# Optimization experiments

Measured on AMD Instinct MI355X. Metric: run time of the kernel, lower is better.

Reference implementation:

```python
import jax, jax.numpy as jnp
import numpy as np

D = 1024      # input_dim / hidden_size
H = 16        # n_heads
HD = D // H   # head_size = 64
F = 4096      # mlp_dim
EPS = 1e-6


def setup_inputs() -> dict:
    key = jax.random.key(0)
    ks = jax.random.split(key, 16)
    s = 0.02
    inp = {
        "x": jax.random.normal(ks[0], (4, 2048, D), dtype=jnp.float32),
        # attention params (torch Linear: y = x @ W.T + b; we store W as [out,in])
        "Wq": jax.random.normal(ks[1], (D, D), dtype=jnp.float32) * s,
        "bq": jax.random.normal(ks[2], (D,), dtype=jnp.float32) * s,
        "Wk": jax.random.normal(ks[3], (D, D), dtype=jnp.float32) * s,
        "bk": jax.random.normal(ks[4], (D,), dtype=jnp.float32) * s,
        "Wv": jax.random.normal(ks[5], (D, D), dtype=jnp.float32) * s,
        "bv": jax.random.normal(ks[6], (D,), dtype=jnp.float32) * s,
        "Wo": jax.random.normal(ks[7], (D, D), dtype=jnp.float32) * s,
        "bo": jax.random.normal(ks[8], (D,), dtype=jnp.float32) * s,
        # MLP params
        "W1": jax.random.normal(ks[9], (F, D), dtype=jnp.float32) * s,
        "b1": jax.random.normal(ks[10], (F,), dtype=jnp.float32) * s,
        "W2": jax.random.normal(ks[11], (D, F), dtype=jnp.float32) * s,
        "b2": jax.random.normal(ks[12], (D,), dtype=jnp.float32) * s,
        # LayerNorm params
        "ln1_g": jnp.ones((D,), dtype=jnp.float32),
        "ln1_b": jnp.zeros((D,), dtype=jnp.float32),
        "ln2_g": jnp.ones((D,), dtype=jnp.float32),
        "ln2_b": jnp.zeros((D,), dtype=jnp.float32),
    }
    return inp


def _layernorm(x, g, b):
    mu = jnp.mean(x, axis=-1, keepdims=True)
    var = jnp.mean(jnp.square(x - mu), axis=-1, keepdims=True)
    return (x - mu) * jax.lax.rsqrt(var + EPS) * g + b


def reference(x, Wq, bq, Wk, bk, Wv, bv, Wo, bo, W1, b1, W2, b2,
              ln1_g, ln1_b, ln2_g, ln2_b):
    B, S, _ = x.shape
    h = x
    xn = _layernorm(x, ln1_g, ln1_b)
    # Q/K/V projections -> [B, H, S, HD]
    def split_heads(t):
        return t.reshape(B, S, H, HD).transpose(0, 2, 1, 3)
    q = split_heads(xn @ Wq.T + bq)
    k = split_heads(xn @ Wk.T + bk)
    v = split_heads(xn @ Wv.T + bv)
    scores = jnp.einsum('bhqd,bhkd->bhqk', q, k) / np.sqrt(HD).astype(np.float32)
    probs = jax.nn.softmax(scores, axis=-1)
    ctx = jnp.einsum('bhqk,bhkd->bhqd', probs, v)      # [B,H,S,HD]
    ctx = ctx.transpose(0, 2, 1, 3).reshape(B, S, D)
    attn_out = ctx @ Wo.T + bo
    x = attn_out + h
    h = x
    xn = _layernorm(x, ln2_g, ln2_b)
    y = jax.nn.gelu(xn @ W1.T + b1, approximate=False)  # torch nn.GELU() = exact erf gelu
    y = y @ W2.T + b2
    return y + h
```

## Files before the change

kernel.cpp:

```cpp
#include <hip/hip_runtime.h>
#include <hip/hip_bf16.h>
#include <math.h>

typedef __attribute__((ext_vector_type(8))) short short8;
typedef __attribute__((ext_vector_type(4))) float f32x4;

#define MFMA_BF16 __builtin_amdgcn_mfma_f32_16x16x32_bf16

__device__ __forceinline__ ushort f2bf(float f) {
  union { __hip_bfloat16 h; ushort u; } c;
  c.h = __float2bfloat16(f);
  return c.u;
}
__device__ __forceinline__ void async_cp16(const ushort* g, ushort* l) {
  __builtin_amdgcn_global_load_lds(
      (const __attribute__((address_space(1))) void*)g,
      (__attribute__((address_space(3))) void*)l, 16, 0, 0);
}

__global__ __launch_bounds__(256) void conv_all(
    const float* __restrict__ Wq, const float* __restrict__ Wk,
    const float* __restrict__ Wv, const float* __restrict__ Wo,
    const float* __restrict__ W1, const float* __restrict__ W2,
    const float* __restrict__ bq, const float* __restrict__ bk,
    const float* __restrict__ bv,
    ushort* __restrict__ wqkv, ushort* __restrict__ wo,
    ushort* __restrict__ w1, ushort* __restrict__ w2,
    float* __restrict__ bqkv) {
  int i = blockIdx.x * 256 + threadIdx.x;
  if (i < 3145728) {
    const float* src; ushort* dst; int off;
    if (i < 786432)        {
      dst = wqkv; off = i;
      if (i < 262144)      src = Wq + (size_t)i * 4;
      else if (i < 524288) src = Wk + (size_t)(i - 262144) * 4;
      else                 src = Wv + (size_t)(i - 524288) * 4;
    } else if (i < 1048576) { dst = wo; off = i - 786432;  src = Wo + (size_t)off * 4; }
    else if (i < 2097152)   { dst = w1; off = i - 1048576; src = W1 + (size_t)off * 4; }
    else                    { dst = w2; off = i - 2097152; src = W2 + (size_t)off * 4; }
    float4 v = *(const float4*)src;
    ushort4 o;
    o.x = f2bf(v.x); o.y = f2bf(v.y); o.z = f2bf(v.z); o.w = f2bf(v.w);
    ((ushort4*)dst)[off] = o;
  } else if (i < 3146496) {
    int off = i - 3145728;
    const float* src;
    if (off < 256)      src = bq + (size_t)off * 4;
    else if (off < 512) src = bk + (size_t)(off - 256) * 4;
    else                src = bv + (size_t)(off - 512) * 4;
    ((float4*)bqkv)[off] = *(const float4*)src;
  }
}

__global__ __launch_bounds__(256) void ln_kernel(const float* __restrict__ x,
    const float* __restrict__ g, const float* __restrict__ b,
    ushort* __restrict__ out) {
  const int row = blockIdx.x, t = threadIdx.x;
  float4 v = ((const float4*)(x + (size_t)row * 1024))[t];
  float s  = v.x + v.y + v.z + v.w;
  float ss = v.x*v.x + v.y*v.y + v.z*v.z + v.w*v.w;
  #pragma unroll
  for (int off = 32; off >= 1; off >>= 1) {
    s  += __shfl_xor(s, off);
    ss += __shfl_xor(ss, off);
  }
  __shared__ float red[8];
  int wv = t >> 6, ln = t & 63;
  if (ln == 0) { red[wv] = s; red[4 + wv] = ss; }
  __syncthreads();
  float S  = red[0] + red[1] + red[2] + red[3];
  float SS = red[4] + red[5] + red[6] + red[7];
  float mu  = S * (1.0f/1024.0f);
  float var = SS * (1.0f/1024.0f) - mu*mu;
  float rs  = rsqrtf(var + 1e-6f);
  float4 gv = ((const float4*)g)[t];
  float4 bv = ((const float4*)b)[t];
  ushort4 o;
  o.x = f2bf((v.x-mu)*rs*gv.x + bv.x);
  o.y = f2bf((v.y-mu)*rs*gv.y + bv.y);
  o.z = f2bf((v.z-mu)*rs*gv.z + bv.z);
  o.w = f2bf((v.w-mu)*rs*gv.w + bv.w);
  ((ushort4*)(out + (size_t)row*1024))[t] = o;
}

enum { EPI_QK = 0, EPI_VT = 1, EPI_WO = 2, EPI_GELU = 3, EPI_OUT = 4 };

template <int EPI>
__global__ __launch_bounds__(256) void gemm_kernel(const ushort* __restrict__ A,
    const ushort* __restrict__ Bw, const float* __restrict__ bias,
    const float* __restrict__ res, void* __restrict__ outp,
    void* __restrict__ outp2, int K, int N, float scale) {
  __shared__ ushort As[2][128 * 32];
  __shared__ ushort Bs[2][128 * 32];
  const int t = threadIdx.x;
  const int m0 = blockIdx.x * 128, n0 = blockIdx.y * 128;
  const int lane = t & 63, wave = t >> 6;
  const int col = lane & 15, quad = lane >> 4;
  const int wrow = (wave >> 1) * 64, wcol = (wave & 1) * 64;

  f32x4 acc[4][4];
  #pragma unroll
  for (int i = 0; i < 4; i++)
    #pragma unroll
    for (int j = 0; j < 4; j++)
      acc[i][j] = (f32x4){0.f, 0.f, 0.f, 0.f};

  const int lrow = lane >> 2, lcol = (lane & 3) * 8;
  const ushort* Ag = A  + (size_t)(m0 + wave * 32 + lrow) * K + lcol;
  const ushort* Bg = Bw + (size_t)(n0 + wave * 32 + lrow) * K + lcol;
  const int ldso = (wave * 32) * 32;

  for (int k0 = 0; k0 < K; k0 += 64) {
    __syncthreads();
    #pragma unroll
    for (int c = 0; c < 2; c++) {
      async_cp16(Ag + k0 + c * 32,                  &As[c][ldso]);
      async_cp16(Ag + (size_t)16 * K + k0 + c * 32, &As[c][ldso + 16 * 32]);
      async_cp16(Bg + k0 + c * 32,                  &Bs[c][ldso]);
      async_cp16(Bg + (size_t)16 * K + k0 + c * 32, &Bs[c][ldso + 16 * 32]);
    }
    __syncthreads();
    #pragma unroll
    for (int c = 0; c < 2; c++) {
      short8 af[4], bf[4];
      #pragma unroll
      for (int tm = 0; tm < 4; tm++)
        af[tm] = *(const short8*)&As[c][(wrow + tm * 16 + col) * 32 + quad * 8];
      #pragma unroll
      for (int tn = 0; tn < 4; tn++)
        bf[tn] = *(const short8*)&Bs[c][(wcol + tn * 16 + col) * 32 + quad * 8];
      #pragma unroll
      for (int tm = 0; tm < 4; tm++)
        #pragma unroll
        for (int tn = 0; tn < 4; tn++)
          acc[tm][tn] = MFMA_BF16(af[tm], bf[tn], acc[tm][tn], 0, 0, 0);
    }
  }

  #pragma unroll
  for (int tm = 0; tm < 4; tm++) {
    #pragma unroll
    for (int tn = 0; tn < 4; tn++) {
      const int n = n0 + wcol + tn * 16 + col;
      const float bn = (EPI == EPI_VT) ? 0.f : bias[n];
      #pragma unroll
      for (int r = 0; r < 4; r++) {
        const int m = m0 + wrow + tm * 16 + quad * 4 + r;
        float v = acc[tm][tn][r] + bn;
        if (EPI == EPI_VT) {
          float vv = v + bias[m];
          int h = m >> 6, hd = m & 63, bb = n >> 11, s2 = n & 2047;
          ((ushort*)outp)[((size_t)((bb * 16 + h) * 64 + hd)) * 2048 + s2] = f2bf(vv);
        } else if (EPI == EPI_GELU) {
          float u = v * 0.7978845608028654f * (1.0f + 0.044715f * v * v);
          float e = __builtin_amdgcn_exp2f(u * 2.885390081777927f);
          float th = 1.0f - 2.0f * __builtin_amdgcn_rcpf(e + 1.0f);
          ((ushort*)outp)[(size_t)m * N + n] = f2bf(0.5f * v * (1.0f + th));
        } else {
          ((float*)outp)[(size_t)m * N + n] = v + res[(size_t)m * N + n];
        }
      }
    }
  }
}

template <int EPI>
__global__ __launch_bounds__(512, 2) void gemm256_kernel(const ushort* __restrict__ A,
    const ushort* __restrict__ Bw, const float* __restrict__ bias,
    void* __restrict__ outp, void* __restrict__ outp2, int K, int N, float scale) {
  __shared__ ushort As[2][256 * 64];
  __shared__ ushort Bs[2][256 * 64];
  const int t = threadIdx.x;
  const int lane = t & 63, wave = t >> 6;
  const int col = lane & 15, quad = lane >> 4;
  const int m0 = blockIdx.x * 256, n0 = blockIdx.y * 256;
  const int wm = wave >> 2, wn = wave & 3;

  f32x4 acc[8][4];
  #pragma unroll
  for (int i = 0; i < 8; i++)
    #pragma unroll
    for (int j = 0; j < 4; j++)
      acc[i][j] = (f32x4){0.f, 0.f, 0.f, 0.f};

  size_t aoff[2], boff[2];
  int d0[2];
  #pragma unroll
  for (int i = 0; i < 2; i++) {
    int c = i * 512 + t, r = c >> 3, p = c & 7;
    aoff[i] = (size_t)(m0 + r) * K + (p ^ (r & 7)) * 8;
    boff[i] = (size_t)(n0 + r) * K + (p ^ (r & 7)) * 8;
    d0[i] = c * 8;
  }
  const size_t up = (size_t)128 * K;

  const int NT = K >> 6;
  #pragma unroll
  for (int i = 0; i < 2; i++) async_cp16(A  + aoff[i],      &As[0][d0[i]]);
  #pragma unroll
  for (int i = 0; i < 2; i++) async_cp16(Bw + boff[i],      &Bs[0][d0[i]]);
  #pragma unroll
  for (int i = 0; i < 2; i++) async_cp16(A  + aoff[i] + up, &As[0][8192 + d0[i]]);
  #pragma unroll
  for (int i = 0; i < 2; i++) async_cp16(Bw + boff[i] + up, &Bs[0][8192 + d0[i]]);
  asm volatile("s_waitcnt vmcnt(4)" ::: "memory");
  __builtin_amdgcn_sched_barrier(0);
  __builtin_amdgcn_s_barrier();
  __builtin_amdgcn_sched_barrier(0);

  short8 af[4][2], bf[2][2];
  for (int kt = 0; kt < NT; kt++) {
    const int cur = kt & 1, nxt = cur ^ 1;
    const size_t ko = (size_t)(kt + 1) << 6;
    const bool more = (kt + 1 < NT);
    #pragma unroll
    for (int ph = 0; ph < 4; ph++) {
      const int ha = ph & 1;
      const int hb = ph >> 1;
      #pragma unroll
      for (int tml = 0; tml < 4; tml++) {
        const int row = ha * 128 + wm * 64 + tml * 16 + col;
        #pragma unroll
        for (int c = 0; c < 2; c++)
          af[tml][c] = *(const short8*)&As[cur][row * 64 + (((c * 4 + quad) ^ (row & 7)) * 8)];
      }
      if (ph == 0 || ph == 2) {
        #pragma unroll
        for (int tnl = 0; tnl < 2; tnl++) {
          const int row = hb * 128 + wn * 32 + tnl * 16 + col;
          #pragma unroll
          for (int c = 0; c < 2; c++)
            bf[tnl][c] = *(const short8*)&Bs[cur][row * 64 + (((c * 4 + quad) ^ (row & 7)) * 8)];
        }
      }
      if (more) {
        if (ph == 0) {
          #pragma unroll
          for (int i = 0; i < 2; i++) async_cp16(A  + aoff[i] + ko,      &As[nxt][d0[i]]);
        } else if (ph == 1) {
          #pragma unroll
          for (int i = 0; i < 2; i++) async_cp16(Bw + boff[i] + ko,      &Bs[nxt][d0[i]]);
        } else if (ph == 2) {
          #pragma unroll
          for (int i = 0; i < 2; i++) async_cp16(A  + aoff[i] + up + ko, &As[nxt][8192 + d0[i]]);
        } else {
          #pragma unroll
          for (int i = 0; i < 2; i++) async_cp16(Bw + boff[i] + up + ko, &Bs[nxt][8192 + d0[i]]);
        }
        asm volatile("s_waitcnt vmcnt(4)" ::: "memory");
      } else {
        if (ph == 0)      asm volatile("s_waitcnt vmcnt(2)" ::: "memory");
        else              asm volatile("s_waitcnt vmcnt(0)" ::: "memory");
      }
      __builtin_amdgcn_sched_barrier(0);
      __builtin_amdgcn_s_barrier();
      asm volatile("s_waitcnt lgkmcnt(0)" ::: "memory");
      __builtin_amdgcn_sched_barrier(0);
      __builtin_amdgcn_s_setprio(1);
      #pragma unroll
      for (int tml = 0; tml < 4; tml++)
        #pragma unroll
        for (int tnl = 0; tnl < 2; tnl++) {
          acc[ha*4+tml][hb*2+tnl] = MFMA_BF16(af[tml][0], bf[tnl][0], acc[ha*4+tml][hb*2+tnl], 0, 0, 0);
          acc[ha*4+tml][hb*2+tnl] = MFMA_BF16(af[tml][1], bf[tnl][1], acc[ha*4+tml][hb*2+tnl], 0, 0, 0);
        }
      __builtin_amdgcn_s_setprio(0);
      __builtin_amdgcn_sched_barrier(0);
      __builtin_amdgcn_s_barrier();
      __builtin_amdgcn_sched_barrier(0);
    }
  }

  #pragma unroll
  for (int tm = 0; tm < 8; tm++) {
    const int ha = tm >> 2, tml = tm & 3;
    #pragma unroll
    for (int tn = 0; tn < 4; tn++) {
      const int hb = tn >> 1, tnl = tn & 1;
      const int n = n0 + hb * 128 + wn * 32 + tnl * 16 + col;
      const float bn = bias[n];
      #pragma unroll
      for (int r = 0; r < 4; r++) {
        const int m = m0 + ha * 128 + wm * 64 + tml * 16 + quad * 4 + r;
        float v = acc[tm][tn][r] + bn;
        if (EPI == EPI_QK) {
          int nl = n & 1023, h = nl >> 6, hd = nl & 63;
          int bb = m >> 11, s2 = m & 2047;
          if (n < 1024)
            ((ushort*)outp)[(((size_t)(bb * 16 + h) * 2048 + s2) * 64) + hd] = f2bf(v * scale);
          else
            ((ushort*)outp2)[(((size_t)(bb * 16 + h) * 2048 + s2) * 64) + hd] = f2bf(v);
        } else {
          float u = v * 0.7978845608028654f * (1.0f + 0.044715f * v * v);
          float e = __builtin_amdgcn_exp2f(u * 2.885390081777927f);
          float th = 1.0f - 2.0f * __builtin_amdgcn_rcpf(e + 1.0f);
          ((ushort*)outp)[(size_t)m * N + n] = f2bf(0.5f * v * (1.0f + th));
        }
      }
    }
  }
}

__global__ __launch_bounds__(256) void attn_kernel(const ushort* __restrict__ Qb,
    const ushort* __restrict__ Kb, const ushort* __restrict__ Vt,
    ushort* __restrict__ ctx) {
  const int lane = threadIdx.x & 63, wave = threadIdx.x >> 6;
  const int col = lane & 15, quad = lane >> 4;
  const int bx = blockIdx.x;
  const int bh = bx & 63;
  const int qt = bx >> 6;
  const int qbase = qt * 128 + wave * 32;
  const ushort* Qh = Qb + (size_t)bh * 2048 * 64;
  const ushort* Kh = Kb + (size_t)bh * 2048 * 64;
  const ushort* Vh = Vt + (size_t)bh * 64 * 2048;

  short8 qa[2][2];
  #pragma unroll
  for (int qg = 0; qg < 2; qg++) {
    const ushort* Qr = Qh + (size_t)(qbase + qg * 16 + col) * 64 + quad * 8;
    qa[qg][0] = *(const short8*)Qr;
    qa[qg][1] = *(const short8*)(Qr + 32);
  }

  f32x4 Ot[2][4];
  float l_part[2];
  #pragma unroll
  for (int qg = 0; qg < 2; qg++) {
    l_part[qg] = 0.f;
    #pragma unroll
    for (int dt = 0; dt < 4; dt++) Ot[qg][dt] = (f32x4){0.f, 0.f, 0.f, 0.f};
  }

  __shared__ ushort Ks[2][2][64 * 32];
  __shared__ ushort Vs[2][2][64 * 32];
  __shared__ ushort P_lds[4][16][64];

  const int lrow = lane >> 2;
  const int srow = wave * 16 + lrow;
  const int lcol = ((lane & 3) ^ ((srow >> 1) & 3)) * 8;
  const ushort* Kg = Kh + (size_t)srow * 64 + lcol;
  const ushort* Vg = Vh + (size_t)srow * 2048 + lcol;
  const int so = (wave * 16) * 32;

  const int kvswz = (col >> 1) & 3;
  const int pswz = col & 7;

  async_cp16(Kg,      &Ks[0][0][so]);
  async_cp16(Kg + 32, &Ks[0][1][so]);
  async_cp16(Vg,      &Vs[0][0][so]);
  async_cp16(Vg + 32, &Vs[0][1][so]);
  __syncthreads();

  int cur = 0;
  for (int kb = 0; kb < 2048; kb += 64) {
    if (kb + 64 < 2048) {
      const int nxt = cur ^ 1;
      async_cp16(Kg + (size_t)(kb + 64) * 64,      &Ks[nxt][0][so]);
      async_cp16(Kg + (size_t)(kb + 64) * 64 + 32, &Ks[nxt][1][so]);
      async_cp16(Vg + (kb + 64),                   &Vs[nxt][0][so]);
      async_cp16(Vg + (kb + 64) + 32,              &Vs[nxt][1][so]);
    }

    short8 kf[4][2], vf[4][2];
    #pragma unroll
    for (int kt = 0; kt < 4; kt++)
      #pragma unroll
      for (int c = 0; c < 2; c++)
        kf[kt][c] = *(const short8*)&Ks[cur][c][(kt * 16 + col) * 32 + (quad ^ kvswz) * 8];
    #pragma unroll
    for (int dt = 0; dt < 4; dt++)
      #pragma unroll
      for (int c = 0; c < 2; c++)
        vf[dt][c] = *(const short8*)&Vs[cur][c][(dt * 16 + col) * 32 + (quad ^ kvswz) * 8];

    #pragma unroll
    for (int qg = 0; qg < 2; qg++) {
      f32x4 s[4];
      __builtin_amdgcn_s_setprio(1);
      #pragma unroll
      for (int kt = 0; kt < 4; kt++) {
        s[kt] = (f32x4){0.f, 0.f, 0.f, 0.f};
        s[kt] = MFMA_BF16(kf[kt][0], qa[qg][0], s[kt], 0, 0, 0);
        s[kt] = MFMA_BF16(kf[kt][1], qa[qg][1], s[kt], 0, 0, 0);
      }
      __builtin_amdgcn_s_setprio(0);
      ushort(*P)[64] = P_lds[wave];
      #pragma unroll
      for (int kt = 0; kt < 4; kt++) {
        float p0 = __builtin_amdgcn_exp2f(s[kt][0]);
        float p1 = __builtin_amdgcn_exp2f(s[kt][1]);
        float p2 = __builtin_amdgcn_exp2f(s[kt][2]);
        float p3 = __builtin_amdgcn_exp2f(s[kt][3]);
        l_part[qg] += (p0 + p1) + (p2 + p3);
        uint2 pk;
        asm("v_cvt_pk_bf16_f32 %0, %1, %2" : "=v"(pk.x) : "v"(p0), "v"(p1));
        asm("v_cvt_pk_bf16_f32 %0, %1, %2" : "=v"(pk.y) : "v"(p2), "v"(p3));
        *(uint2*)&P[col][(((2 * kt + (quad >> 1)) ^ pswz) * 8) + (quad & 1) * 4] = pk;
      }
      #pragma unroll
      for (int c = 0; c < 2; c++) {
        short8 pf = *(const short8*)&P_lds[wave][col][((4 * c + quad) ^ pswz) * 8];
        __builtin_amdgcn_s_setprio(1);
        #pragma unroll
        for (int dt = 0; dt < 4; dt++)
          Ot[qg][dt] = MFMA_BF16(vf[dt][c], pf, Ot[qg][dt], 0, 0, 0);
        __builtin_amdgcn_s_setprio(0);
      }
    }
    __syncthreads();
    cur ^= 1;
  }

  const int bb = bh >> 4, h = bh & 15;
  #pragma unroll
  for (int qg = 0; qg < 2; qg++) {
    float l = l_part[qg];
    l += __shfl_xor(l, 16);
    l += __shfl_xor(l, 32);
    float inv = __builtin_amdgcn_rcpf(l);
    const int q = qbase + qg * 16 + col;
    size_t base = ((size_t)(bb * 2048 + q)) * 1024 + h * 64;
    #pragma unroll
    for (int dt = 0; dt < 4; dt++) {
      ushort4 o;
      o.x = f2bf(Ot[qg][dt][0] * inv);
      o.y = f2bf(Ot[qg][dt][1] * inv);
      o.z = f2bf(Ot[qg][dt][2] * inv);
      o.w = f2bf(Ot[qg][dt][3] * inv);
      *(ushort4*)&ctx[base + dt * 16 + quad * 4] = o;
    }
  }
}

extern "C" void kernel_launch(void* const* d_in, const int* in_sizes, int n_in,
                              void* d_out, int out_size, void* d_ws, size_t ws_size,
                              hipStream_t stream) {
  const float* x     = (const float*)d_in[0];
  const float* Wq    = (const float*)d_in[1];
  const float* bq    = (const float*)d_in[2];
  const float* Wk    = (const float*)d_in[3];
  const float* bk    = (const float*)d_in[4];
  const float* Wv    = (const float*)d_in[5];
  const float* bv    = (const float*)d_in[6];
  const float* Wo    = (const float*)d_in[7];
  const float* bo    = (const float*)d_in[8];
  const float* W1    = (const float*)d_in[9];
  const float* b1    = (const float*)d_in[10];
  const float* W2    = (const float*)d_in[11];
  const float* b2    = (const float*)d_in[12];
  const float* ln1_g = (const float*)d_in[13];
  const float* ln1_b = (const float*)d_in[14];
  const float* ln2_g = (const float*)d_in[15];
  const float* ln2_b = (const float*)d_in[16];

  const size_t MB = 1ull << 20;
  char* ws = (char*)d_ws;
  ushort* Wqkv_b = (ushort*)(ws + 0 * MB);
  ushort* Wo_b   = (ushort*)(ws + 6 * MB);
  ushort* W1_b   = (ushort*)(ws + 8 * MB);
  ushort* W2_b   = (ushort*)(ws + 16 * MB);
  ushort* xn1    = (ushort*)(ws + 24 * MB);
  ushort* Qb     = (ushort*)(ws + 40 * MB);
  ushort* Kb     = (ushort*)(ws + 56 * MB);
  ushort* Vt     = (ushort*)(ws + 72 * MB);
  ushort* ctxb   = (ushort*)(ws + 88 * MB);
  float*  x2     = (float*)(ws + 104 * MB);
  ushort* xn2    = (ushort*)(ws + 136 * MB);
  ushort* y1     = (ushort*)(ws + 152 * MB);
  float*  bqkv   = (float*)(ws + 152 * MB);

  conv_all<<<12291, 256, 0, stream>>>(Wq, Wk, Wv, Wo, W1, W2, bq, bk, bv,
                                      Wqkv_b, Wo_b, W1_b, W2_b, bqkv);

  ln_kernel<<<8192, 256, 0, stream>>>(x, ln1_g, ln1_b, xn1);

  const float cs = 0.125f * 1.4426950408889634f;
  gemm256_kernel<EPI_QK><<<dim3(32, 8), 512, 0, stream>>>(
      xn1, Wqkv_b, bqkv, Qb, Kb, 1024, 2048, cs);
  gemm_kernel<EPI_VT><<<dim3(8, 64), 256, 0, stream>>>(
      Wqkv_b + (size_t)2048 * 1024, xn1, bqkv + 2048, nullptr, Vt, nullptr,
      1024, 8192, 1.0f);

  attn_kernel<<<1024, 256, 0, stream>>>(Qb, Kb, Vt, ctxb);

  gemm_kernel<EPI_WO><<<dim3(64, 8), 256, 0, stream>>>(
      ctxb, Wo_b, bo, x, x2, nullptr, 1024, 1024, 1.0f);

  ln_kernel<<<8192, 256, 0, stream>>>(x2, ln2_g, ln2_b, xn2);

  gemm256_kernel<EPI_GELU><<<dim3(32, 16), 512, 0, stream>>>(
      xn2, W1_b, b1, y1, nullptr, 1024, 4096, 1.0f);
  gemm_kernel<EPI_OUT><<<dim3(64, 8), 256, 0, stream>>>(
      y1, W2_b, b2, x2, d_out, nullptr, 4096, 1024, 1.0f);
}
```

Measured before the change: 510.3 us.

## Replace 128x128 GEMMs with pipelined 256x128 kernel and compute softmax sum via MFMA

Replaces the simple double-sync 128x128 GEMM used for V-projection, Wo and W2 with a new 256x128, 512-thread kernel. It uses swizzled LDS, staged async prefetch of the next K-tile interleaved with MFMA phases, and setprio. The 256x256 GEMM's phase loop is manually unrolled so the A fragments of both halves stay in registers instead of being reloaded from LDS. In attention, the row-sum of probabilities is now taken with an extra MFMA against a vector of ones rather than scalar adds plus shuffles. This costs an extra matrix instruction per step, and the sum is formed from bf16-rounded probabilities.

```diff
diff --git a/kernel.cpp b/kernel.cpp
--- a/kernel.cpp
+++ b/kernel.cpp
@@ -86,85 +86,6 @@
 enum { EPI_QK = 0, EPI_VT = 1, EPI_WO = 2, EPI_GELU = 3, EPI_OUT = 4 };
 
 template <int EPI>
-__global__ __launch_bounds__(256) void gemm_kernel(const ushort* __restrict__ A,
-    const ushort* __restrict__ Bw, const float* __restrict__ bias,
-    const float* __restrict__ res, void* __restrict__ outp,
-    void* __restrict__ outp2, int K, int N, float scale) {
-  __shared__ ushort As[2][128 * 32];
-  __shared__ ushort Bs[2][128 * 32];
-  const int t = threadIdx.x;
-  const int m0 = blockIdx.x * 128, n0 = blockIdx.y * 128;
-  const int lane = t & 63, wave = t >> 6;
-  const int col = lane & 15, quad = lane >> 4;
-  const int wrow = (wave >> 1) * 64, wcol = (wave & 1) * 64;
-
-  f32x4 acc[4][4];
-  #pragma unroll
-  for (int i = 0; i < 4; i++)
-    #pragma unroll
-    for (int j = 0; j < 4; j++)
-      acc[i][j] = (f32x4){0.f, 0.f, 0.f, 0.f};
-
-  const int lrow = lane >> 2, lcol = (lane & 3) * 8;
-  const ushort* Ag = A  + (size_t)(m0 + wave * 32 + lrow) * K + lcol;
-  const ushort* Bg = Bw + (size_t)(n0 + wave * 32 + lrow) * K + lcol;
-  const int ldso = (wave * 32) * 32;
-
-  for (int k0 = 0; k0 < K; k0 += 64) {
-    __syncthreads();
-    #pragma unroll
-    for (int c = 0; c < 2; c++) {
-      async_cp16(Ag + k0 + c * 32,                  &As[c][ldso]);
-      async_cp16(Ag + (size_t)16 * K + k0 + c * 32, &As[c][ldso + 16 * 32]);
-      async_cp16(Bg + k0 + c * 32,                  &Bs[c][ldso]);
-      async_cp16(Bg + (size_t)16 * K + k0 + c * 32, &Bs[c][ldso + 16 * 32]);
-    }
-    __syncthreads();
-    #pragma unroll
-    for (int c = 0; c < 2; c++) {
-      short8 af[4], bf[4];
-      #pragma unroll
-      for (int tm = 0; tm < 4; tm++)
-        af[tm] = *(const short8*)&As[c][(wrow + tm * 16 + col) * 32 + quad * 8];
-      #pragma unroll
-      for (int tn = 0; tn < 4; tn++)
-        bf[tn] = *(const short8*)&Bs[c][(wcol + tn * 16 + col) * 32 + quad * 8];
-      #pragma unroll
-      for (int tm = 0; tm < 4; tm++)
-        #pragma unroll
-        for (int tn = 0; tn < 4; tn++)
-          acc[tm][tn] = MFMA_BF16(af[tm], bf[tn], acc[tm][tn], 0, 0, 0);
-    }
-  }
-
-  #pragma unroll
-  for (int tm = 0; tm < 4; tm++) {
-    #pragma unroll
-    for (int tn = 0; tn < 4; tn++) {
-      const int n = n0 + wcol + tn * 16 + col;
-      const float bn = (EPI == EPI_VT) ? 0.f : bias[n];
-      #pragma unroll
-      for (int r = 0; r < 4; r++) {
-        const int m = m0 + wrow + tm * 16 + quad * 4 + r;
-        float v = acc[tm][tn][r] + bn;
-        if (EPI == EPI_VT) {
-          float vv = v + bias[m];
-          int h = m >> 6, hd = m & 63, bb = n >> 11, s2 = n & 2047;
-          ((ushort*)outp)[((size_t)((bb * 16 + h) * 64 + hd)) * 2048 + s2] = f2bf(vv);
-        } else if (EPI == EPI_GELU) {
-          float u = v * 0.7978845608028654f * (1.0f + 0.044715f * v * v);
-          float e = __builtin_amdgcn_exp2f(u * 2.885390081777927f);
-          float th = 1.0f - 2.0f * __builtin_amdgcn_rcpf(e + 1.0f);
-          ((ushort*)outp)[(size_t)m * N + n] = f2bf(0.5f * v * (1.0f + th));
-        } else {
-          ((float*)outp)[(size_t)m * N + n] = v + res[(size_t)m * N + n];
-        }
-      }
-    }
-  }
-}
-
-template <int EPI>
 __global__ __launch_bounds__(512, 2) void gemm256_kernel(const ushort* __restrict__ A,
     const ushort* __restrict__ Bw, const float* __restrict__ bias,
     void* __restrict__ outp, void* __restrict__ outp2, int K, int N, float scale) {
@@ -208,67 +129,135 @@
   __builtin_amdgcn_s_barrier();
   __builtin_amdgcn_sched_barrier(0);
 
-  short8 af[4][2], bf[2][2];
+  short8 af0[4][2], af1[4][2], bf[2][2];
   for (int kt = 0; kt < NT; kt++) {
     const int cur = kt & 1, nxt = cur ^ 1;
     const size_t ko = (size_t)(kt + 1) << 6;
     const bool more = (kt + 1 < NT);
-    #pragma unroll
-    for (int ph = 0; ph < 4; ph++) {
-      const int ha = ph & 1;
-      const int hb = ph >> 1;
-      #pragma unroll
-      for (int tml = 0; tml < 4; tml++) {
-        const int row = ha * 128 + wm * 64 + tml * 16 + col;
-        #pragma unroll
-        for (int c = 0; c < 2; c++)
-          af[tml][c] = *(const short8*)&As[cur][row * 64 + (((c * 4 + quad) ^ (row & 7)) * 8)];
-      }
-      if (ph == 0 || ph == 2) {
-        #pragma unroll
-        for (int tnl = 0; tnl < 2; tnl++) {
-          const int row = hb * 128 + wn * 32 + tnl * 16 + col;
-          #pragma unroll
-          for (int c = 0; c < 2; c++)
-            bf[tnl][c] = *(const short8*)&Bs[cur][row * 64 + (((c * 4 + quad) ^ (row & 7)) * 8)];
-        }
-      }
-      if (more) {
-        if (ph == 0) {
-          #pragma unroll
-          for (int i = 0; i < 2; i++) async_cp16(A  + aoff[i] + ko,      &As[nxt][d0[i]]);
-        } else if (ph == 1) {
-          #pragma unroll
-          for (int i = 0; i < 2; i++) async_cp16(Bw + boff[i] + ko,      &Bs[nxt][d0[i]]);
-        } else if (ph == 2) {
-          #pragma unroll
-          for (int i = 0; i < 2; i++) async_cp16(A  + aoff[i] + up + ko, &As[nxt][8192 + d0[i]]);
-        } else {
-          #pragma unroll
-          for (int i = 0; i < 2; i++) async_cp16(Bw + boff[i] + up + ko, &Bs[nxt][8192 + d0[i]]);
-        }
-        asm volatile("s_waitcnt vmcnt(4)" ::: "memory");
-      } else {
-        if (ph == 0)      asm volatile("s_waitcnt vmcnt(2)" ::: "memory");
-        else              asm volatile("s_waitcnt vmcnt(0)" ::: "memory");
-      }
-      __builtin_amdgcn_sched_barrier(0);
-      __builtin_amdgcn_s_barrier();
-      asm volatile("s_waitcnt lgkmcnt(0)" ::: "memory");
-      __builtin_amdgcn_sched_barrier(0);
-      __builtin_amdgcn_s_setprio(1);
-      #pragma unroll
-      for (int tml = 0; tml < 4; tml++)
-        #pragma unroll
-        for (int tnl = 0; tnl < 2; tnl++) {
-          acc[ha*4+tml][hb*2+tnl] = MFMA_BF16(af[tml][0], bf[tnl][0], acc[ha*4+tml][hb*2+tnl], 0, 0, 0);
-          acc[ha*4+tml][hb*2+tnl] = MFMA_BF16(af[tml][1], bf[tnl][1], acc[ha*4+tml][hb*2+tnl], 0, 0, 0);
-        }
-      __builtin_amdgcn_s_setprio(0);
-      __builtin_amdgcn_sched_barrier(0);
-      __builtin_amdgcn_s_barrier();
-      __builtin_amdgcn_sched_barrier(0);
-    }
+
+    #pragma unroll
+    for (int tml = 0; tml < 4; tml++) {
+      const int row = wm * 64 + tml * 16 + col;
+      #pragma unroll
+      for (int c = 0; c < 2; c++)
+        af0[tml][c] = *(const short8*)&As[cur][row * 64 + (((c * 4 + quad) ^ (row & 7)) * 8)];
+    }
+    #pragma unroll
+    for (int tnl = 0; tnl < 2; tnl++) {
+      const int row = wn * 32 + tnl * 16 + col;
+      #pragma unroll
+      for (int c = 0; c < 2; c++)
+        bf[tnl][c] = *(const short8*)&Bs[cur][row * 64 + (((c * 4 + quad) ^ (row & 7)) * 8)];
+    }
+    if (more) {
+      #pragma unroll
+      for (int i = 0; i < 2; i++) async_cp16(A + aoff[i] + ko, &As[nxt][d0[i]]);
+      asm volatile("s_waitcnt vmcnt(4)" ::: "memory");
+    } else {
+      asm volatile("s_waitcnt vmcnt(2)" ::: "memory");
+    }
+    __builtin_amdgcn_sched_barrier(0);
+    __builtin_amdgcn_s_barrier();
+    asm volatile("s_waitcnt lgkmcnt(0)" ::: "memory");
+    __builtin_amdgcn_sched_barrier(0);
+    __builtin_amdgcn_s_setprio(1);
+    #pragma unroll
+    for (int tml = 0; tml < 4; tml++)
+      #pragma unroll
+      for (int tnl = 0; tnl < 2; tnl++) {
+        acc[tml][tnl] = MFMA_BF16(af0[tml][0], bf[tnl][0], acc[tml][tnl], 0, 0, 0);
+        acc[tml][tnl] = MFMA_BF16(af0[tml][1], bf[tnl][1], acc[tml][tnl], 0, 0, 0);
+      }
+    __builtin_amdgcn_s_setprio(0);
+    __builtin_amdgcn_sched_barrier(0);
+    __builtin_amdgcn_s_barrier();
+    __builtin_amdgcn_sched_barrier(0);
+
+    #pragma unroll
+    for (int tml = 0; tml < 4; tml++) {
+      const int row = 128 + wm * 64 + tml * 16 + col;
+      #pragma unroll
+      for (int c = 0; c < 2; c++)
+        af1[tml][c] = *(const short8*)&As[cur][row * 64 + (((c * 4 + quad) ^ (row & 7)) * 8)];
+    }
+    if (more) {
+      #pragma unroll
+      for (int i = 0; i < 2; i++) async_cp16(Bw + boff[i] + ko, &Bs[nxt][d0[i]]);
+      asm volatile("s_waitcnt vmcnt(4)" ::: "memory");
+    } else {
+      asm volatile("s_waitcnt vmcnt(0)" ::: "memory");
+    }
+    __builtin_amdgcn_sched_barrier(0);
+    __builtin_amdgcn_s_barrier();
+    asm volatile("s_waitcnt lgkmcnt(0)" ::: "memory");
+    __builtin_amdgcn_sched_barrier(0);
+    __builtin_amdgcn_s_setprio(1);
+    #pragma unroll
+    for (int tml = 0; tml < 4; tml++)
+      #pragma unroll
+      for (int tnl = 0; tnl < 2; tnl++) {
+        acc[4+tml][tnl] = MFMA_BF16(af1[tml][0], bf[tnl][0], acc[4+tml][tnl], 0, 0, 0);
+        acc[4+tml][tnl] = MFMA_BF16(af1[tml][1], bf[tnl][1], acc[4+tml][tnl], 0, 0, 0);
+      }
+    __builtin_amdgcn_s_setprio(0);
+    __builtin_amdgcn_sched_barrier(0);
+    __builtin_amdgcn_s_barrier();
+    __builtin_amdgcn_sched_barrier(0);
+
+    #pragma unroll
+    for (int tnl = 0; tnl < 2; tnl++) {
+      const int row = 128 + wn * 32 + tnl * 16 + col;
+      #pragma unroll
+      for (int c = 0; c < 2; c++)
+        bf[tnl][c] = *(const short8*)&Bs[cur][row * 64 + (((c * 4 + quad) ^ (row & 7)) * 8)];
+    }
+    if (more) {
+      #pragma unroll
+      for (int i = 0; i < 2; i++) async_cp16(A + aoff[i] + up + ko, &As[nxt][8192 + d0[i]]);
+      asm volatile("s_waitcnt vmcnt(4)" ::: "memory");
+    } else {
+      asm volatile("s_waitcnt vmcnt(0)" ::: "memory");
+    }
+    __builtin_amdgcn_sched_barrier(0);
+    __builtin_amdgcn_s_barrier();
+    asm volatile("s_waitcnt lgkmcnt(0)" ::: "memory");
+    __builtin_amdgcn_sched_barrier(0);
+    __builtin_amdgcn_s_setprio(1);
+    #pragma unroll
+    for (int tml = 0; tml < 4; tml++)
+      #pragma unroll
+      for (int tnl = 0; tnl < 2; tnl++) {
+        acc[tml][2+tnl] = MFMA_BF16(af0[tml][0], bf[tnl][0], acc[tml][2+tnl], 0, 0, 0);
+        acc[tml][2+tnl] = MFMA_BF16(af0[tml][1], bf[tnl][1], acc[tml][2+tnl], 0, 0, 0);
+      }
+    __builtin_amdgcn_s_setprio(0);
+    __builtin_amdgcn_sched_barrier(0);
+    __builtin_amdgcn_s_barrier();
+    __builtin_amdgcn_sched_barrier(0);
+
+    if (more) {
+      #pragma unroll
+      for (int i = 0; i < 2; i++) async_cp16(Bw + boff[i] + up + ko, &Bs[nxt][8192 + d0[i]]);
+      asm volatile("s_waitcnt vmcnt(4)" ::: "memory");
+    } else {
+      asm volatile("s_waitcnt vmcnt(0)" ::: "memory");
+    }
+    __builtin_amdgcn_sched_barrier(0);
+    __builtin_amdgcn_s_barrier();
+    asm volatile("s_waitcnt lgkmcnt(0)" ::: "memory");
+    __builtin_amdgcn_sched_barrier(0);
+    __builtin_amdgcn_s_setprio(1);
+    #pragma unroll
+    for (int tml = 0; tml < 4; tml++)
+      #pragma unroll
+      for (int tnl = 0; tnl < 2; tnl++) {
+        acc[4+tml][2+tnl] = MFMA_BF16(af1[tml][0], bf[tnl][0], acc[4+tml][2+tnl], 0, 0, 0);
+        acc[4+tml][2+tnl] = MFMA_BF16(af1[tml][1], bf[tnl][1], acc[4+tml][2+tnl], 0, 0, 0);
+      }
+    __builtin_amdgcn_s_setprio(0);
+    __builtin_amdgcn_sched_barrier(0);
+    __builtin_amdgcn_s_barrier();
+    __builtin_amdgcn_sched_barrier(0);
   }
 
   #pragma unroll
@@ -301,6 +290,207 @@
   }
 }
 
+template <int EPI>
+__global__ __launch_bounds__(512, 2) void gemmW_kernel(const ushort* __restrict__ A,
+    const ushort* __restrict__ Bw, const float* __restrict__ bias,
+    const float* __restrict__ res, void* __restrict__ outp, int K, int N) {
+  __shared__ ushort As[2][256 * 64];
+  __shared__ ushort Bs[2][128 * 64];
+  const int t = threadIdx.x;
+  const int lane = t & 63, wave = t >> 6;
+  const int col = lane & 15, quad = lane >> 4;
+  const int m0 = blockIdx.x * 256, n0 = blockIdx.y * 128;
+  const int wm = wave >> 1, wn = wave & 1;
+
+  f32x4 acc[4][4];
+  #pragma unroll
+  for (int i = 0; i < 4; i++)
+    #pragma unroll
+    for (int j = 0; j < 4; j++)
+      acc[i][j] = (f32x4){0.f, 0.f, 0.f, 0.f};
+
+  size_t aoff[2];
+  int ad0[2];
+  #pragma unroll
+  for (int i = 0; i < 2; i++) {
+    int c = i * 512 + t, r = c >> 3, p = c & 7;
+    aoff[i] = (size_t)(m0 + r) * K + (p ^ (r & 7)) * 8;
+    ad0[i] = c * 8;
+  }
+  size_t boff;
+  int bd0;
+  {
+    int c = t, r = c >> 3, p = c & 7;
+    boff = (size_t)(n0 + r) * K + (p ^ (r & 7)) * 8;
+    bd0 = c * 8;
+  }
+  const size_t upA = (size_t)128 * K;
+  const size_t upB = (size_t)64 * K;
+
+  const int NT = K >> 6;
+  #pragma unroll
+  for (int i = 0; i < 2; i++) async_cp16(A + aoff[i], &As[0][ad0[i]]);
+  async_cp16(Bw + boff, &Bs[0][bd0]);
+  #pragma unroll
+  for (int i = 0; i < 2; i++) async_cp16(A + aoff[i] + upA, &As[0][8192 + ad0[i]]);
+  async_cp16(Bw + boff + upB, &Bs[0][4096 + bd0]);
+  asm volatile("s_waitcnt vmcnt(3)" ::: "memory");
+  __builtin_amdgcn_sched_barrier(0);
+  __builtin_amdgcn_s_barrier();
+  __builtin_amdgcn_sched_barrier(0);
+
+  short8 af0[2][2], af1[2][2], bf[2][2];
+  for (int kt = 0; kt < NT; kt++) {
+    const int cur = kt & 1, nxt = cur ^ 1;
+    const size_t ko = (size_t)(kt + 1) << 6;
+    const bool more = (kt + 1 < NT);
+
+    #pragma unroll
+    for (int tml = 0; tml < 2; tml++) {
+      const int row = wm * 32 + tml * 16 + col;
+      #pragma unroll
+      for (int c = 0; c < 2; c++)
+        af0[tml][c] = *(const short8*)&As[cur][row * 64 + (((c * 4 + quad) ^ (row & 7)) * 8)];
+    }
+    #pragma unroll
+    for (int tnl = 0; tnl < 2; tnl++) {
+      const int row = wn * 32 + tnl * 16 + col;
+      #pragma unroll
+      for (int c = 0; c < 2; c++)
+        bf[tnl][c] = *(const short8*)&Bs[cur][row * 64 + (((c * 4 + quad) ^ (row & 7)) * 8)];
+    }
+    if (more) {
+      #pragma unroll
+      for (int i = 0; i < 2; i++) async_cp16(A + aoff[i] + ko, &As[nxt][ad0[i]]);
+      asm volatile("s_waitcnt vmcnt(3)" ::: "memory");
+    } else {
+      asm volatile("s_waitcnt vmcnt(1)" ::: "memory");
+    }
+    __builtin_amdgcn_sched_barrier(0);
+    __builtin_amdgcn_s_barrier();
+    asm volatile("s_waitcnt lgkmcnt(0)" ::: "memory");
+    __builtin_amdgcn_sched_barrier(0);
+    __builtin_amdgcn_s_setprio(1);
+    #pragma unroll
+    for (int tml = 0; tml < 2; tml++)
+      #pragma unroll
+      for (int tnl = 0; tnl < 2; tnl++) {
+        acc[tml][tnl] = MFMA_BF16(af0[tml][0], bf[tnl][0], acc[tml][tnl], 0, 0, 0);
+        acc[tml][tnl] = MFMA_BF16(af0[tml][1], bf[tnl][1], acc[tml][tnl], 0, 0, 0);
+      }
+    __builtin_amdgcn_s_setprio(0);
+    __builtin_amdgcn_sched_barrier(0);
+    __builtin_amdgcn_s_barrier();
+    __builtin_amdgcn_sched_barrier(0);
+
+    #pragma unroll
+    for (int tml = 0; tml < 2; tml++) {
+      const int row = 128 + wm * 32 + tml * 16 + col;
+      #pragma unroll
+      for (int c = 0; c < 2; c++)
+        af1[tml][c] = *(const short8*)&As[cur][row * 64 + (((c * 4 + quad) ^ (row & 7)) * 8)];
+    }
+    if (more) {
+      async_cp16(Bw + boff + ko, &Bs[nxt][bd0]);
+      asm volatile("s_waitcnt vmcnt(3)" ::: "memory");
+    } else {
+      asm volatile("s_waitcnt vmcnt(0)" ::: "memory");
+    }
+    __builtin_amdgcn_sched_barrier(0);
+    __builtin_amdgcn_s_barrier();
+    asm volatile("s_waitcnt lgkmcnt(0)" ::: "memory");
+    __builtin_amdgcn_sched_barrier(0);
+    __builtin_amdgcn_s_setprio(1);
+    #pragma unroll
+    for (int tml = 0; tml < 2; tml++)
+      #pragma unroll
+      for (int tnl = 0; tnl < 2; tnl++) {
+        acc[2+tml][tnl] = MFMA_BF16(af1[tml][0], bf[tnl][0], acc[2+tml][tnl], 0, 0, 0);
+        acc[2+tml][tnl] = MFMA_BF16(af1[tml][1], bf[tnl][1], acc[2+tml][tnl], 0, 0, 0);
+      }
+    __builtin_amdgcn_s_setprio(0);
+    __builtin_amdgcn_sched_barrier(0);
+    __builtin_amdgcn_s_barrier();
+    __builtin_amdgcn_sched_barrier(0);
+
+    #pragma unroll
+    for (int tnl = 0; tnl < 2; tnl++) {
+      const int row = 64 + wn * 32 + tnl * 16 + col;
+      #pragma unroll
+      for (int c = 0; c < 2; c++)
+        bf[tnl][c] = *(const short8*)&Bs[cur][4096 + ((row - 64) * 64) + (((c * 4 + quad) ^ (row & 7)) * 8)];
+    }
+    if (more) {
+      #pragma unroll
+      for (int i = 0; i < 2; i++) async_cp16(A + aoff[i] + upA + ko, &As[nxt][8192 + ad0[i]]);
+      asm volatile("s_waitcnt vmcnt(5)" ::: "memory");
+    } else {
+      asm volatile("s_waitcnt vmcnt(0)" ::: "memory");
+    }
+    __builtin_amdgcn_sched_barrier(0);
+    __builtin_amdgcn_s_barrier();
+    asm volatile("s_waitcnt lgkmcnt(0)" ::: "memory");
+    __builtin_amdgcn_sched_barrier(0);
+    __builtin_amdgcn_s_setprio(1);
+    #pragma unroll
+    for (int tml = 0; tml < 2; tml++)
+      #pragma unroll
+      for (int tnl = 0; tnl < 2; tnl++) {
+        acc[tml][2+tnl] = MFMA_BF16(af0[tml][0], bf[tnl][0], acc[tml][2+tnl], 0, 0, 0);
+        acc[tml][2+tnl] = MFMA_BF16(af0[tml][1], bf[tnl][1], acc[tml][2+tnl], 0, 0, 0);
+      }
+    __builtin_amdgcn_s_setprio(0);
+    __builtin_amdgcn_sched_barrier(0);
+    __builtin_amdgcn_s_barrier();
+    __builtin_amdgcn_sched_barrier(0);
+
+    if (more) {
+      async_cp16(Bw + boff + upB + ko, &Bs[nxt][4096 + bd0]);
+      asm volatile("s_waitcnt vmcnt(3)" ::: "memory");
+    } else {
+      asm volatile("s_waitcnt vmcnt(0)" ::: "memory");
+    }
+    __builtin_amdgcn_sched_barrier(0);
+    __builtin_amdgcn_s_barrier();
+    asm volatile("s_waitcnt lgkmcnt(0)" ::: "memory");
+    __builtin_amdgcn_sched_barrier(0);
+    __builtin_amdgcn_s_setprio(1);
+    #pragma unroll
+    for (int tml = 0; tml < 2; tml++)
+      #pragma unroll
+      for (int tnl = 0; tnl < 2; tnl++) {
+        acc[2+tml][2+tnl] = MFMA_BF16(af1[tml][0], bf[tnl][0], acc[2+tml][2+tnl], 0, 0, 0);
+        acc[2+tml][2+tnl] = MFMA_BF16(af1[tml][1], bf[tnl][1], acc[2+tml][2+tnl], 0, 0, 0);
+      }
+    __builtin_amdgcn_s_setprio(0);
+    __builtin_amdgcn_sched_barrier(0);
+    __builtin_amdgcn_s_barrier();
+    __builtin_amdgcn_sched_barrier(0);
+  }
+
+  #pragma unroll
+  for (int tm = 0; tm < 4; tm++) {
+    const int ha = tm >> 1, tml = tm & 1;
+    #pragma unroll
+    for (int tn = 0; tn < 4; tn++) {
+      const int hb = tn >> 1, tnl = tn & 1;
+      const int n = n0 + hb * 64 + wn * 32 + tnl * 16 + col;
+      #pragma unroll
+      for (int r = 0; r < 4; r++) {
+        const int m = m0 + ha * 128 + wm * 32 + tml * 16 + quad * 4 + r;
+        float v = acc[tm][tn][r];
+        if (EPI == EPI_VT) {
+          float vv = v + bias[m];
+          int h = m >> 6, hd = m & 63, bb = n >> 11, s2 = n & 2047;
+          ((ushort*)outp)[((size_t)((bb * 16 + h) * 64 + hd)) * 2048 + s2] = f2bf(vv);
+        } else {
+          ((float*)outp)[(size_t)m * N + n] = v + bias[n] + res[(size_t)m * N + n];
+        }
+      }
+    }
+  }
+}
+
 __global__ __launch_bounds__(256) void attn_kernel(const ushort* __restrict__ Qb,
     const ushort* __restrict__ Kb, const ushort* __restrict__ Vt,
     ushort* __restrict__ ctx) {
@@ -322,11 +512,14 @@
     qa[qg][1] = *(const short8*)(Qr + 32);
   }
 
-  f32x4 Ot[2][4];
-  float l_part[2];
+  short8 ones8;
+  #pragma unroll
+  for (int i = 0; i < 8; i++) ones8[i] = (short)0x3F80;
+
+  f32x4 Ot[2][4], Ol[2];
   #pragma unroll
   for (int qg = 0; qg < 2; qg++) {
-    l_part[qg] = 0.f;
+    Ol[qg] = (f32x4){0.f, 0.f, 0.f, 0.f};
     #pragma unroll
     for (int dt = 0; dt < 4; dt++) Ot[qg][dt] = (f32x4){0.f, 0.f, 0.f, 0.f};
   }
@@ -391,7 +584,6 @@
         float p1 = __builtin_amdgcn_exp2f(s[kt][1]);
         float p2 = __builtin_amdgcn_exp2f(s[kt][2]);
         float p3 = __builtin_amdgcn_exp2f(s[kt][3]);
-        l_part[qg] += (p0 + p1) + (p2 + p3);
         uint2 pk;
         asm("v_cvt_pk_bf16_f32 %0, %1, %2" : "=v"(pk.x) : "v"(p0), "v"(p1));
         asm("v_cvt_pk_bf16_f32 %0, %1, %2" : "=v"(pk.y) : "v"(p2), "v"(p3));
@@ -404,6 +596,7 @@
         #pragma unroll
         for (int dt = 0; dt < 4; dt++)
           Ot[qg][dt] = MFMA_BF16(vf[dt][c], pf, Ot[qg][dt], 0, 0, 0);
+        Ol[qg] = MFMA_BF16(ones8, pf, Ol[qg], 0, 0, 0);
         __builtin_amdgcn_s_setprio(0);
       }
     }
@@ -414,10 +607,7 @@
   const int bb = bh >> 4, h = bh & 15;
   #pragma unroll
   for (int qg = 0; qg < 2; qg++) {
-    float l = l_part[qg];
-    l += __shfl_xor(l, 16);
-    l += __shfl_xor(l, 32);
-    float inv = __builtin_amdgcn_rcpf(l);
+    float inv = __builtin_amdgcn_rcpf(Ol[qg][0]);
     const int q = qbase + qg * 16 + col;
     size_t base = ((size_t)(bb * 2048 + q)) * 1024 + h * 64;
     #pragma unroll
@@ -477,19 +667,18 @@
   const float cs = 0.125f * 1.4426950408889634f;
   gemm256_kernel<EPI_QK><<<dim3(32, 8), 512, 0, stream>>>(
       xn1, Wqkv_b, bqkv, Qb, Kb, 1024, 2048, cs);
-  gemm_kernel<EPI_VT><<<dim3(8, 64), 256, 0, stream>>>(
-      Wqkv_b + (size_t)2048 * 1024, xn1, bqkv + 2048, nullptr, Vt, nullptr,
-      1024, 8192, 1.0f);
+  gemmW_kernel<EPI_VT><<<dim3(4, 64), 512, 0, stream>>>(
+      Wqkv_b + (size_t)2048 * 1024, xn1, bqkv + 2048, nullptr, Vt, 1024, 8192);
 
   attn_kernel<<<1024, 256, 0, stream>>>(Qb, Kb, Vt, ctxb);
 
-  gemm_kernel<EPI_WO><<<dim3(64, 8), 256, 0, stream>>>(
-      ctxb, Wo_b, bo, x, x2, nullptr, 1024, 1024, 1.0f);
+  gemmW_kernel<EPI_WO><<<dim3(32, 8), 512, 0, stream>>>(
+      ctxb, Wo_b, bo, x, x2, 1024, 1024);
 
   ln_kernel<<<8192, 256, 0, stream>>>(x2, ln2_g, ln2_b, xn2);
 
   gemm256_kernel<EPI_GELU><<<dim3(32, 16), 512, 0, stream>>>(
       xn2, W1_b, b1, y1, nullptr, 1024, 4096, 1.0f);
-  gemm_kernel<EPI_OUT><<<dim3(64, 8), 256, 0, stream>>>(
-      y1, W2_b, b2, x2, d_out, nullptr, 4096, 1024, 1.0f);
-}
+  gemmW_kernel<EPI_OUT><<<dim3(32, 8), 512, 0, stream>>>(
+      y1, W2_b, b2, x2, d_out, 4096, 1024);
+}
```

Result: no change. 518.6 us (+1.6%).
